# Kernel tuning notes

Hardware: AMD Instinct MI355X
Metric: run time of the kernel (lower is better)

## Reference

```python
import jax, jax.numpy as jnp
import numpy as np

N = 100000
E = 1600000
D_IN = 64
D_H = 64
D_OUT = 10
EPS_BN = 1e-5
EPS_NORM = 1e-12


def setup_inputs() -> dict:
    key = jax.random.key(0)
    ks = jax.random.split(key, 16)
    x = jax.random.normal(ks[0], (N, D_IN), dtype=jnp.float32)
    edge_index = jax.random.randint(ks[1], (2, E), 0, N, dtype=jnp.int64)
    def lin(k, fo, fi):
        s = 1.0 / np.sqrt(fi)
        return jax.random.uniform(k, (fo, fi), jnp.float32, -s, s)
    return {
        "x": x, "edge_index": edge_index,
        "Wl1": lin(ks[2], D_H, D_IN), "Wr1": lin(ks[3], D_H, D_IN), "b1": jnp.zeros((D_H,), jnp.float32),
        "g1": jnp.ones((D_H,), jnp.float32), "be1": jnp.zeros((D_H,), jnp.float32),
        "Wl2": lin(ks[4], D_H, D_H), "Wr2": lin(ks[5], D_H, D_H), "b2": jnp.zeros((D_H,), jnp.float32),
        "g2": jnp.ones((D_H,), jnp.float32), "be2": jnp.zeros((D_H,), jnp.float32),
        "Wl3": lin(ks[6], D_OUT, D_H), "Wr3": lin(ks[7], D_OUT, D_H), "b3": jnp.zeros((D_OUT,), jnp.float32),
    }


def _sage_conv(x, src, dst, Wl, Wr, b, normalize):
    # mean aggregation over incoming edges (messages flow src -> dst)
    agg = jax.ops.segment_sum(x[src], dst, num_segments=N)
    cnt = jax.ops.segment_sum(jnp.ones((src.shape[0],), x.dtype), dst, num_segments=N)
    mean = agg / jnp.clip(cnt, 1.0)[:, None]
    out = mean @ Wl.T + x @ Wr.T + b
    if normalize:
        nrm = jnp.sqrt(jnp.sum(out * out, axis=-1, keepdims=True))
        out = out / jnp.maximum(nrm, EPS_NORM)
    return out


def _batchnorm(x, gamma, beta):
    mu = jnp.mean(x, axis=0)
    var = jnp.mean((x - mu) ** 2, axis=0)  # biased var (training mode)
    return (x - mu) * jax.lax.rsqrt(var + EPS_BN) * gamma + beta


def reference(x, edge_index, Wl1, Wr1, b1, g1, be1, Wl2, Wr2, b2, g2, be2, Wl3, Wr3, b3):
    src, dst = edge_index[0], edge_index[1]
    h = _sage_conv(x, src, dst, Wl1, Wr1, b1, True)
    h = jax.nn.relu(_batchnorm(h, g1, be1))
    h = _sage_conv(h, src, dst, Wl2, Wr2, b2, True)
    h = jax.nn.relu(_batchnorm(h, g2, be2))
    h = _sage_conv(h, src, dst, Wl3, Wr3, b3, False)
    return h
```

## Files before the change

kernel.cpp:

```cpp
#include <hip/hip_runtime.h>
#include <hip/hip_bf16.h>

#define NN 100000
#define EE 1600000
#define BSZ 512
#define NBKT 196
#define CHUNK 8192
#define NCH 196

typedef short bf16x8 __attribute__((ext_vector_type(8)));
typedef float f32x4 __attribute__((ext_vector_type(4)));
typedef float f32x2 __attribute__((ext_vector_type(2)));

__device__ inline unsigned short bf16_of(float f) {
    __hip_bfloat16 h = __float2bfloat16(f);
    return *reinterpret_cast<unsigned short*>(&h);
}
__device__ inline unsigned pack2(float a, float b) {
    return (unsigned)bf16_of(a) | ((unsigned)bf16_of(b) << 16);
}
__device__ inline float bflo(unsigned u) { return __uint_as_float(u << 16); }
__device__ inline float bfhi(unsigned u) { return __uint_as_float(u & 0xffff0000u); }
__device__ inline f32x2 unpk2(unsigned u) {
    f32x2 r; r.x = __uint_as_float(u << 16); r.y = __uint_as_float(u & 0xffff0000u);
    return r;
}


__global__ __launch_bounds__(256)
void k_ccount(const int* __restrict__ ei, int* __restrict__ ccount) {
    __shared__ int hist[NBKT];
    int tid = threadIdx.x;
    int e0 = blockIdx.x * CHUNK;
    int e1 = e0 + CHUNK; if (e1 > EE) e1 = EE;
    for (int i = tid; i < NBKT; i += 256) hist[i] = 0;
    __syncthreads();
    for (int e = e0 + tid; e < e1; e += 256)
        atomicAdd(&hist[ei[EE + e] >> 9], 1);
    __syncthreads();
    for (int i = tid; i < NBKT; i += 256)
        if (hist[i]) atomicAdd(&ccount[i], hist[i]);
}

__global__ void k_cscan(const int* __restrict__ ccount, int* __restrict__ cbase,
                        int* __restrict__ gcur) {
    __shared__ int s[256];
    int tid = threadIdx.x;
    int v = (tid < NBKT) ? ccount[tid] : 0;
    s[tid] = v;
    __syncthreads();
    for (int off = 1; off < 256; off <<= 1) {
        int t = (tid >= off) ? s[tid - off] : 0;
        __syncthreads();
        if (tid >= off) s[tid] += t;
        __syncthreads();
    }
    if (tid < NBKT) {
        int excl = s[tid] - v;
        cbase[tid] = excl;
        gcur[tid] = excl;
    }
    if (tid == NBKT - 1) cbase[NBKT] = s[tid];
}

__global__ __launch_bounds__(256)
void k_coarse(const int* __restrict__ ei, int* __restrict__ gcur, int* __restrict__ pairs) {
    __shared__ int hist[NBKT];
    __shared__ int base[NBKT];
    __shared__ int curs[NBKT];
    int tid = threadIdx.x;
    int e0 = blockIdx.x * CHUNK;
    int e1 = e0 + CHUNK; if (e1 > EE) e1 = EE;
    for (int i = tid; i < NBKT; i += 256) hist[i] = 0;
    __syncthreads();
    for (int e = e0 + tid; e < e1; e += 256)
        atomicAdd(&hist[ei[EE + e] >> 9], 1);
    __syncthreads();
    for (int i = tid; i < NBKT; i += 256) {
        base[i] = atomicAdd(&gcur[i], hist[i]);
        curs[i] = 0;
    }
    __syncthreads();
    for (int e = e0 + tid; e < e1; e += 256) {
        int src = ei[e];
        int dst = ei[EE + e];
        int b = dst >> 9;
        int off = atomicAdd(&curs[b], 1);
        pairs[base[b] + off] = (src << 9) | (dst & 511);
    }
}

__global__ __launch_bounds__(512)
void k_fine(const int* __restrict__ cbase, const int* __restrict__ pairs,
            int* __restrict__ rs, int* __restrict__ esrc) {
    __shared__ int deg[BSZ];
    __shared__ int s[BSZ];
    int b = blockIdx.x;
    int n0 = b * BSZ;
    int nlocal = NN - n0; if (nlocal > BSZ) nlocal = BSZ;
    int tid = threadIdx.x;
    deg[tid] = 0;
    __syncthreads();
    int e0 = cbase[b], e1 = cbase[b + 1];
    for (int e = e0 + tid; e < e1; e += 512)
        atomicAdd(&deg[pairs[e] & 511], 1);
    __syncthreads();
    int v = deg[tid];
    s[tid] = v;
    __syncthreads();
    for (int off = 1; off < 512; off <<= 1) {
        int t = (tid >= off) ? s[tid - off] : 0;
        __syncthreads();
        if (tid >= off) s[tid] += t;
        __syncthreads();
    }
    int excl = s[tid] - v;
    if (tid < nlocal) rs[n0 + tid] = e0 + excl;
    if (b == NBKT - 1 && tid == 0) rs[NN] = EE;
    deg[tid] = e0 + excl;
    __syncthreads();
    for (int e = e0 + tid; e < e1; e += 512) {
        int pk = pairs[e];
        int pos = atomicAdd(&deg[pk & 511], 1);
        esrc[pos] = pk >> 9;
    }
}

__global__ __launch_bounds__(256)
void k_tobfW(const float4* __restrict__ src, ushort4* __restrict__ dst,
             const float* __restrict__ Wl1, const float* __restrict__ Wr1,
             const float* __restrict__ Wl2, const float* __restrict__ Wr2,
             unsigned short* __restrict__ w1, unsigned short* __restrict__ w2,
             int* __restrict__ ccount) {
    int b = blockIdx.x, tid = threadIdx.x;
    if (b < 6250) {
        int i = b * 256 + tid;
        if (i < NN * 16) {
            float4 v = src[i];
            dst[i] = make_ushort4(bf16_of(v.x), bf16_of(v.y), bf16_of(v.z), bf16_of(v.w));
        }
    } else {
        for (int i = tid; i < 8192; i += 256) {
            int n = i >> 7, k = i & 127;
            float v1 = (k < 64) ? Wl1[n * 64 + k] : Wr1[n * 64 + (k - 64)];
            w1[i] = bf16_of(v1);
            float v2 = (k < 64) ? Wl2[n * 64 + k] : Wr2[n * 64 + (k - 64)];
            w2[i] = bf16_of(v2);
        }
        if (tid < NBKT) ccount[tid] = 0;
    }
}

__global__ __launch_bounds__(256, 8)
void k_aggbf(const unsigned short* __restrict__ xbf, const int* __restrict__ rs,
             const int* __restrict__ esrc, unsigned short* __restrict__ meanbf,
             const float* __restrict__ sc, const float* __restrict__ sh) {
    const int tid = threadIdx.x;
    const int node = blockIdx.x * 32 + (tid >> 3);
    if (node >= NN) return;
    const int c = tid & 7;
    const int s0 = rs[node], s1 = rs[node + 1];
    const uint4* xb = (const uint4*)xbf;
    f32x2 a0 = {0.f, 0.f}, a1 = a0, a2 = a0, a3 = a0;
    if (sc) {
        const f32x2* sc2 = (const f32x2*)sc;
        const f32x2* sh2 = (const f32x2*)sh;
        const f32x2 s0v = sc2[4 * c + 0], s1v = sc2[4 * c + 1];
        const f32x2 s2v = sc2[4 * c + 2], s3v = sc2[4 * c + 3];
        const f32x2 h0v = sh2[4 * c + 0], h1v = sh2[4 * c + 1];
        const f32x2 h2v = sh2[4 * c + 2], h3v = sh2[4 * c + 3];
        const f32x2 z = {0.f, 0.f};
#define ACCS(v) do { \
        a0 += __builtin_elementwise_max(__builtin_elementwise_fma(unpk2((v).x), s0v, h0v), z); \
        a1 += __builtin_elementwise_max(__builtin_elementwise_fma(unpk2((v).y), s1v, h1v), z); \
        a2 += __builtin_elementwise_max(__builtin_elementwise_fma(unpk2((v).z), s2v, h2v), z); \
        a3 += __builtin_elementwise_max(__builtin_elementwise_fma(unpk2((v).w), s3v, h3v), z); \
        } while (0)
        int p = s0;
        for (; p + 3 < s1; p += 4) {
            int e0 = esrc[p], e1 = esrc[p + 1], e2 = esrc[p + 2], e3 = esrc[p + 3];
            uint4 v0 = xb[(size_t)e0 * 8 + c];
            uint4 v1 = xb[(size_t)e1 * 8 + c];
            uint4 v2 = xb[(size_t)e2 * 8 + c];
            uint4 v3 = xb[(size_t)e3 * 8 + c];
            ACCS(v0); ACCS(v1); ACCS(v2); ACCS(v3);
        }
        for (; p < s1; ++p) {
            uint4 v = xb[(size_t)esrc[p] * 8 + c];
            ACCS(v);
        }
#undef ACCS
    } else {
#define ACCA(v) do { \
        a0 += unpk2((v).x); a1 += unpk2((v).y); \
        a2 += unpk2((v).z); a3 += unpk2((v).w); } while (0)
        int p = s0;
        for (; p + 3 < s1; p += 4) {
            int e0 = esrc[p], e1 = esrc[p + 1], e2 = esrc[p + 2], e3 = esrc[p + 3];
            uint4 v0 = xb[(size_t)e0 * 8 + c];
            uint4 v1 = xb[(size_t)e1 * 8 + c];
            uint4 v2 = xb[(size_t)e2 * 8 + c];
            uint4 v3 = xb[(size_t)e3 * 8 + c];
            ACCA(v0); ACCA(v1); ACCA(v2); ACCA(v3);
        }
        for (; p < s1; ++p) {
            uint4 v = xb[(size_t)esrc[p] * 8 + c];
            ACCA(v);
        }
#undef ACCA
    }
    int cnt = s1 - s0; if (cnt < 1) cnt = 1;
    float inv = 1.0f / (float)cnt;
    uint4 o;
    o.x = pack2(a0.x * inv, a0.y * inv);
    o.y = pack2(a1.x * inv, a1.y * inv);
    o.z = pack2(a2.x * inv, a2.y * inv);
    o.w = pack2(a3.x * inv, a3.y * inv);
    ((uint4*)meanbf)[(size_t)node * 8 + c] = o;
}

__global__ __launch_bounds__(256, 4)
void k_sagemfma(const unsigned short* __restrict__ meanbf,
                const unsigned short* __restrict__ a2bf,
                const unsigned short* __restrict__ Wbf,
                const float* __restrict__ bias,
                unsigned short* __restrict__ outbf,
                float* __restrict__ partials,
                const float* __restrict__ sc, const float* __restrict__ sh) {
    __shared__ float sblk[64];
    __shared__ float qblk[64];
    const int tid = threadIdx.x;
    const int base = blockIdx.x * 64;
    const int col = tid & 15;
    const int q   = (tid >> 4) & 3;
    const int w   = tid >> 6;

    if (tid < 64) { sblk[tid] = 0.f; qblk[tid] = 0.f; }

    int gn = base + w * 16 + col; if (gn > NN - 1) gn = NN - 1;
    const uint4* mb = (const uint4*)meanbf;
    const uint4* ab = (const uint4*)a2bf;
    const uint4* wb = (const uint4*)Wbf;

    uint4 fa0 = mb[gn * 8 + q];
    uint4 fa1 = mb[gn * 8 + 4 + q];
    uint4 fa2 = ab[gn * 8 + q];
    uint4 fa3 = ab[gn * 8 + 4 + q];
    if (sc) {
        float4 s0 = ((const float4*)sc)[q * 2],     s1 = ((const float4*)sc)[q * 2 + 1];
        float4 h0 = ((const float4*)sh)[q * 2],     h1 = ((const float4*)sh)[q * 2 + 1];
        float4 s2 = ((const float4*)sc)[8 + q * 2], s3 = ((const float4*)sc)[8 + q * 2 + 1];
        float4 h2 = ((const float4*)sh)[8 + q * 2], h3 = ((const float4*)sh)[8 + q * 2 + 1];
        fa2.x = pack2(fmaxf(fmaf(bflo(fa2.x), s0.x, h0.x), 0.f),
                      fmaxf(fmaf(bfhi(fa2.x), s0.y, h0.y), 0.f));
        fa2.y = pack2(fmaxf(fmaf(bflo(fa2.y), s0.z, h0.z), 0.f),
                      fmaxf(fmaf(bfhi(fa2.y), s0.w, h0.w), 0.f));
        fa2.z = pack2(fmaxf(fmaf(bflo(fa2.z), s1.x, h1.x), 0.f),
                      fmaxf(fmaf(bfhi(fa2.z), s1.y, h1.y), 0.f));
        fa2.w = pack2(fmaxf(fmaf(bflo(fa2.w), s1.z, h1.z), 0.f),
                      fmaxf(fmaf(bfhi(fa2.w), s1.w, h1.w), 0.f));
        fa3.x = pack2(fmaxf(fmaf(bflo(fa3.x), s2.x, h2.x), 0.f),
                      fmaxf(fmaf(bfhi(fa3.x), s2.y, h2.y), 0.f));
        fa3.y = pack2(fmaxf(fmaf(bflo(fa3.y), s2.z, h2.z), 0.f),
                      fmaxf(fmaf(bfhi(fa3.y), s2.w, h2.w), 0.f));
        fa3.z = pack2(fmaxf(fmaf(bflo(fa3.z), s3.x, h3.x), 0.f),
                      fmaxf(fmaf(bfhi(fa3.z), s3.y, h3.y), 0.f));
        fa3.w = pack2(fmaxf(fmaf(bflo(fa3.w), s3.z, h3.z), 0.f),
                      fmaxf(fmaf(bfhi(fa3.w), s3.w, h3.w), 0.f));
    }
    uint4 fa[4] = {fa0, fa1, fa2, fa3};

    f32x4 acc0 = {0.f, 0.f, 0.f, 0.f}, acc1 = acc0, acc2 = acc0, acc3 = acc0;
#pragma unroll
    for (int c = 0; c < 4; ++c) {
        uint4 b0 = wb[(0 * 16 + col) * 16 + c * 4 + q];
        uint4 b1 = wb[(1 * 16 + col) * 16 + c * 4 + q];
        uint4 b2 = wb[(2 * 16 + col) * 16 + c * 4 + q];
        uint4 b3 = wb[(3 * 16 + col) * 16 + c * 4 + q];
        bf16x8 a = *(const bf16x8*)&fa[c];
        acc0 = __builtin_amdgcn_mfma_f32_16x16x32_bf16(a, *(const bf16x8*)&b0, acc0, 0, 0, 0);
        acc1 = __builtin_amdgcn_mfma_f32_16x16x32_bf16(a, *(const bf16x8*)&b1, acc1, 0, 0, 0);
        acc2 = __builtin_amdgcn_mfma_f32_16x16x32_bf16(a, *(const bf16x8*)&b2, acc2, 0, 0, 0);
        acc3 = __builtin_amdgcn_mfma_f32_16x16x32_bf16(a, *(const bf16x8*)&b3, acc3, 0, 0, 0);
    }

    float bb0 = bias[col], bb1 = bias[16 + col], bb2 = bias[32 + col], bb3 = bias[48 + col];
    float sj0 = 0.f, sj1 = 0.f, sj2 = 0.f, sj3 = 0.f;
    float qj0 = 0.f, qj1 = 0.f, qj2 = 0.f, qj3 = 0.f;
#pragma unroll
    for (int r = 0; r < 4; ++r) {
        int go = base + w * 16 + q * 4 + r;
        float o0 = acc0[r] + bb0, o1 = acc1[r] + bb1;
        float o2 = acc2[r] + bb2, o3 = acc3[r] + bb3;
        float ssv = o0 * o0 + o1 * o1 + o2 * o2 + o3 * o3;
        ssv += __shfl_xor(ssv, 1, 64);
        ssv += __shfl_xor(ssv, 2, 64);
        ssv += __shfl_xor(ssv, 4, 64);
        ssv += __shfl_xor(ssv, 8, 64);
        float inv = 1.0f / fmaxf(sqrtf(ssv), 1e-12f);
        o0 *= inv; o1 *= inv; o2 *= inv; o3 *= inv;
        if (go < NN) {
            outbf[go * 64 + col]      = bf16_of(o0);
            outbf[go * 64 + 16 + col] = bf16_of(o1);
            outbf[go * 64 + 32 + col] = bf16_of(o2);
            outbf[go * 64 + 48 + col] = bf16_of(o3);
            sj0 += o0; sj1 += o1; sj2 += o2; sj3 += o3;
            qj0 += o0 * o0; qj1 += o1 * o1; qj2 += o2 * o2; qj3 += o3 * o3;
        }
    }
#pragma unroll
    for (int m = 16; m <= 32; m <<= 1) {
        sj0 += __shfl_xor(sj0, m, 64); sj1 += __shfl_xor(sj1, m, 64);
        sj2 += __shfl_xor(sj2, m, 64); sj3 += __shfl_xor(sj3, m, 64);
        qj0 += __shfl_xor(qj0, m, 64); qj1 += __shfl_xor(qj1, m, 64);
        qj2 += __shfl_xor(qj2, m, 64); qj3 += __shfl_xor(qj3, m, 64);
    }
    __syncthreads();
    if (q == 0) {
        atomicAdd(&sblk[col], sj0);      atomicAdd(&qblk[col], qj0);
        atomicAdd(&sblk[16 + col], sj1); atomicAdd(&qblk[16 + col], qj1);
        atomicAdd(&sblk[32 + col], sj2); atomicAdd(&qblk[32 + col], qj2);
        atomicAdd(&sblk[48 + col], sj3); atomicAdd(&qblk[48 + col], qj3);
    }
    __syncthreads();
    if (tid < 128)
        partials[blockIdx.x * 128 + tid] = (tid < 64) ? sblk[tid] : qblk[tid - 64];
}

__global__ __launch_bounds__(256)
void k_bnred(const float* __restrict__ partials, int nblk, float* __restrict__ red) {
    __shared__ float s[256];
    int tid = threadIdx.x;
    int idx = tid & 127, half = tid >> 7;
    float a0 = 0.f, a1 = 0.f, a2 = 0.f, a3 = 0.f;
    int r = blockIdx.x * 2 + half;
    for (; r + 192 < nblk; r += 256) {
        a0 += partials[r * 128 + idx];
        a1 += partials[(r + 64) * 128 + idx];
        a2 += partials[(r + 128) * 128 + idx];
        a3 += partials[(r + 192) * 128 + idx];
    }
    for (; r < nblk; r += 64) a0 += partials[r * 128 + idx];
    s[tid] = (a0 + a1) + (a2 + a3);
    __syncthreads();
    if (tid < 128) red[blockIdx.x * 128 + tid] = s[tid] + s[tid + 128];
}

__global__ void k_bnfin(const float* __restrict__ red,
                        const float* __restrict__ g, const float* __restrict__ be,
                        float* __restrict__ scale, float* __restrict__ shift) {
    __shared__ float s[256];
    int tid = threadIdx.x;
    int idx = tid & 127, half = tid >> 7;
    float a = 0.f;
#pragma unroll
    for (int r = half; r < 32; r += 2)
        a += red[r * 128 + idx];
    s[tid] = a;
    __syncthreads();
    if (tid < 128) s[tid] += s[tid + 128];
    __syncthreads();
    if (tid < 64) {
        float mu = s[tid] / (float)NN;
        float var = s[64 + tid] / (float)NN - mu * mu;
        var = fmaxf(var, 0.0f);
        float sc = g[tid] / sqrtf(var + 1e-5f);
        scale[tid] = sc;
        shift[tid] = be[tid] - mu * sc;
    }
}

__global__ __launch_bounds__(256)
void k_project(const unsigned short* __restrict__ h,
               const float* __restrict__ sc, const float* __restrict__ sh,
               const float* __restrict__ Wl, const float* __restrict__ Wr,
               const float* __restrict__ bias,
               float* __restrict__ zl, float* __restrict__ zr) {
    __shared__ float Alds[64 * 128];
    __shared__ float Wlds[64 * 32];
    const int tid = threadIdx.x;
    const int base = blockIdx.x * 128;

#pragma unroll
    for (int i = 0; i < 8; ++i) {
        int idx = i * 256 + tid;
        int f = idx & 31, k = idx >> 5;
        float v = 0.0f;
        if (f < 16) { if (f < 10) v = Wl[f * 64 + k]; }
        else        { if (f - 16 < 10) v = Wr[(f - 16) * 64 + k]; }
        Wlds[k * 32 + f] = v;
    }
    {
        const uint4* h4 = (const uint4*)h;
        const float4* sc4p = (const float4*)sc;
        const float4* sh4p = (const float4*)sh;
#pragma unroll
        for (int i = 0; i < 4; ++i) {
            int idx = i * 256 + tid;
            int node = idx & 127, cb = idx >> 7;
            int gn = base + node; if (gn > NN - 1) gn = NN - 1;
            uint4 u = h4[gn * 8 + cb];
            float4 sA = sc4p[cb * 2], sB = sc4p[cb * 2 + 1];
            float4 hA = sh4p[cb * 2], hB = sh4p[cb * 2 + 1];
            int k0 = cb * 8;
            Alds[(k0 + 0) * 128 + node] = fmaxf(fmaf(bflo(u.x), sA.x, hA.x), 0.f);
            Alds[(k0 + 1) * 128 + node] = fmaxf(fmaf(bfhi(u.x), sA.y, hA.y), 0.f);
            Alds[(k0 + 2) * 128 + node] = fmaxf(fmaf(bflo(u.y), sA.z, hA.z), 0.f);
            Alds[(k0 + 3) * 128 + node] = fmaxf(fmaf(bfhi(u.y), sA.w, hA.w), 0.f);
            Alds[(k0 + 4) * 128 + node] = fmaxf(fmaf(bflo(u.z), sB.x, hB.x), 0.f);
            Alds[(k0 + 5) * 128 + node] = fmaxf(fmaf(bfhi(u.z), sB.y, hB.y), 0.f);
            Alds[(k0 + 6) * 128 + node] = fmaxf(fmaf(bflo(u.w), sB.z, hB.z), 0.f);
            Alds[(k0 + 7) * 128 + node] = fmaxf(fmaf(bfhi(u.w), sB.w, hB.w), 0.f);
        }
    }
    __syncthreads();

    const int fg = tid & 7;
    const int ng = tid >> 3;

    float acc[4][4] = {};
#pragma unroll 4
    for (int k = 0; k < 64; ++k) {
        const float4 a = *(const float4*)(Alds + k * 128 + (ng << 2));
        const float4 w = *(const float4*)(Wlds + k * 32 + (fg << 2));
        const float av[4] = {a.x, a.y, a.z, a.w};
        const float wv[4] = {w.x, w.y, w.z, w.w};
#pragma unroll
        for (int i = 0; i < 4; ++i)
#pragma unroll
            for (int j = 0; j < 4; ++j)
                acc[i][j] = fmaf(av[i], wv[j], acc[i][j]);
    }

    if (fg == 3 || fg == 7) return;
    float4* dst = (fg < 4) ? (float4*)zl : (float4*)zr;
    int fq = (fg < 4) ? fg : fg - 4;
    float bx = 0.f, by = 0.f, bz = 0.f, bw = 0.f;
    if (fg >= 4) {
        int f0 = fq * 4;
        bx = (f0 + 0 < 10) ? bias[f0 + 0] : 0.f;
        by = (f0 + 1 < 10) ? bias[f0 + 1] : 0.f;
        bz = (f0 + 2 < 10) ? bias[f0 + 2] : 0.f;
        bw = (f0 + 3 < 10) ? bias[f0 + 3] : 0.f;
    }
#pragma unroll
    for (int i = 0; i < 4; ++i) {
        int gn = base + (ng << 2) + i;
        if (gn < NN)
            dst[gn * 3 + fq] = make_float4(acc[i][0] + bx, acc[i][1] + by,
                                           acc[i][2] + bz, acc[i][3] + bw);
    }
}

__global__ __launch_bounds__(256)
void k_agg10(const int* __restrict__ rs, const int* __restrict__ esrc,
             const float* __restrict__ zl, const float* __restrict__ zr,
             float* __restrict__ out) {
    int gid = blockIdx.x * 256 + threadIdx.x;
    unsigned node = (unsigned)gid / 3u;
    int j = gid - (int)node * 3;
    if (node >= NN) return;
    int s0 = rs[node], s1 = rs[node + 1];
    const float4* zl4 = (const float4*)zl;
    float4 acc = make_float4(0.f, 0.f, 0.f, 0.f);
    int p = s0;
    for (; p + 3 < s1; p += 4) {
        float4 v0 = zl4[esrc[p] * 3 + j];
        float4 v1 = zl4[esrc[p + 1] * 3 + j];
        float4 v2 = zl4[esrc[p + 2] * 3 + j];
        float4 v3 = zl4[esrc[p + 3] * 3 + j];
        acc.x += (v0.x + v1.x) + (v2.x + v3.x);
        acc.y += (v0.y + v1.y) + (v2.y + v3.y);
        acc.z += (v0.z + v1.z) + (v2.z + v3.z);
        acc.w += (v0.w + v1.w) + (v2.w + v3.w);
    }
    for (; p < s1; ++p) {
        float4 v = zl4[esrc[p] * 3 + j];
        acc.x += v.x; acc.y += v.y; acc.z += v.z; acc.w += v.w;
    }
    int cnt = s1 - s0; if (cnt < 1) cnt = 1;
    float inv = 1.0f / (float)cnt;
    float4 r = ((const float4*)zr)[node * 3 + j];
    r.x = fmaf(acc.x, inv, r.x); r.y = fmaf(acc.y, inv, r.y);
    r.z = fmaf(acc.z, inv, r.z); r.w = fmaf(acc.w, inv, r.w);
    float2* o2 = (float2*)(out + (size_t)node * 10);
    if (j < 2) {
        o2[j * 2 + 0] = make_float2(r.x, r.y);
        o2[j * 2 + 1] = make_float2(r.z, r.w);
    } else {
        o2[4] = make_float2(r.x, r.y);
    }
}


extern "C" void kernel_launch(void* const* d_in, const int* in_sizes, int n_in,
                              void* d_out, int out_size, void* d_ws, size_t ws_size,
                              hipStream_t stream) {
    const float* x   = (const float*)d_in[0];
    const int*   ei  = (const int*)d_in[1];
    const float* Wl1 = (const float*)d_in[2];
    const float* Wr1 = (const float*)d_in[3];
    const float* b1  = (const float*)d_in[4];
    const float* g1  = (const float*)d_in[5];
    const float* be1 = (const float*)d_in[6];
    const float* Wl2 = (const float*)d_in[7];
    const float* Wr2 = (const float*)d_in[8];
    const float* b2  = (const float*)d_in[9];
    const float* g2  = (const float*)d_in[10];
    const float* be2 = (const float*)d_in[11];
    const float* Wl3 = (const float*)d_in[12];
    const float* Wr3 = (const float*)d_in[13];
    const float* b3  = (const float*)d_in[14];
    float* out = (float*)d_out;

    char* w = (char*)d_ws;
    auto alloc = [&](size_t bytes) -> void* {
        void* p = (void*)w;
        w += (bytes + 255) & ~(size_t)255;
        return p;
    };
    int*   ccount = (int*)alloc(256 * 4);
    int*   cbase  = (int*)alloc(256 * 4);
    int*   gcur   = (int*)alloc(256 * 4);
    int*   rs     = (int*)alloc((size_t)(NN + 1) * 4);
    int*   esrc   = (int*)alloc((size_t)EE * 4);
    float* scratch= (float*)alloc((size_t)NN * 64 * 4);
    unsigned short* xbf    = (unsigned short*)alloc((size_t)NN * 64 * 2);
    unsigned short* h1bf   = (unsigned short*)alloc((size_t)NN * 64 * 2);
    unsigned short* meanbf = (unsigned short*)alloc((size_t)NN * 64 * 2);
    unsigned short* wbf1   = (unsigned short*)alloc(8192 * 2);
    unsigned short* wbf2   = (unsigned short*)alloc(8192 * 2);
    float* partials = (float*)alloc((size_t)1563 * 128 * 4);
    float* red    = (float*)alloc(32 * 128 * 4);
    float* scsh   = (float*)alloc(256 * 4);
    int*   pairs  = (int*)scratch;
    float* zl     = scratch;
    float* zr     = scratch + (size_t)NN * 12;

    k_tobfW<<<6251, 256, 0, stream>>>((const float4*)x, (ushort4*)xbf,
                                      Wl1, Wr1, Wl2, Wr2, wbf1, wbf2, ccount);
    k_ccount<<<NCH, 256, 0, stream>>>(ei, ccount);
    k_cscan<<<1, 256, 0, stream>>>(ccount, cbase, gcur);
    k_coarse<<<NCH, 256, 0, stream>>>(ei, gcur, pairs);
    k_fine<<<NBKT, 512, 0, stream>>>(cbase, pairs, rs, esrc);

    const int aggBlocks  = (NN + 31) / 32;
    const int sageBlocks = (NN + 63) / 64;
    const int projBlocks = (NN + 127) / 128;
    const int a10Blocks  = (NN * 3 + 255) / 256;

    k_aggbf<<<aggBlocks, 256, 0, stream>>>(xbf, rs, esrc, meanbf, nullptr, nullptr);
    k_sagemfma<<<sageBlocks, 256, 0, stream>>>(meanbf, xbf, wbf1, b1, h1bf,
                                               partials, nullptr, nullptr);
    k_bnred<<<32, 256, 0, stream>>>(partials, sageBlocks, red);
    k_bnfin<<<1, 256, 0, stream>>>(red, g1, be1, scsh + 0, scsh + 64);

    k_aggbf<<<aggBlocks, 256, 0, stream>>>(h1bf, rs, esrc, meanbf, scsh + 0, scsh + 64);
    k_sagemfma<<<sageBlocks, 256, 0, stream>>>(meanbf, h1bf, wbf2, b2, xbf,
                                               partials, scsh + 0, scsh + 64);
    k_bnred<<<32, 256, 0, stream>>>(partials, sageBlocks, red);
    k_bnfin<<<1, 256, 0, stream>>>(red, g2, be2, scsh + 128, scsh + 192);

    k_project<<<projBlocks, 256, 0, stream>>>(xbf, scsh + 128, scsh + 192,
                                              Wl3, Wr3, b3, zl, zr);
    k_agg10<<<a10Blocks, 256, 0, stream>>>(rs, esrc, zl, zr, out);
}
```

Baseline: 317.0 us.

## Fuse neighbor mean aggregation into the SAGE MFMA kernel

Result: no change. 320.5 us (+1.1%).

```diff
diff --git a/kernel.cpp b/kernel.cpp
--- a/kernel.cpp
+++ b/kernel.cpp
@@ -151,82 +151,15 @@
     }
 }
 
-__global__ __launch_bounds__(256, 8)
-void k_aggbf(const unsigned short* __restrict__ xbf, const int* __restrict__ rs,
-             const int* __restrict__ esrc, unsigned short* __restrict__ meanbf,
-             const float* __restrict__ sc, const float* __restrict__ sh) {
-    const int tid = threadIdx.x;
-    const int node = blockIdx.x * 32 + (tid >> 3);
-    if (node >= NN) return;
-    const int c = tid & 7;
-    const int s0 = rs[node], s1 = rs[node + 1];
-    const uint4* xb = (const uint4*)xbf;
-    f32x2 a0 = {0.f, 0.f}, a1 = a0, a2 = a0, a3 = a0;
-    if (sc) {
-        const f32x2* sc2 = (const f32x2*)sc;
-        const f32x2* sh2 = (const f32x2*)sh;
-        const f32x2 s0v = sc2[4 * c + 0], s1v = sc2[4 * c + 1];
-        const f32x2 s2v = sc2[4 * c + 2], s3v = sc2[4 * c + 3];
-        const f32x2 h0v = sh2[4 * c + 0], h1v = sh2[4 * c + 1];
-        const f32x2 h2v = sh2[4 * c + 2], h3v = sh2[4 * c + 3];
-        const f32x2 z = {0.f, 0.f};
-#define ACCS(v) do { \
-        a0 += __builtin_elementwise_max(__builtin_elementwise_fma(unpk2((v).x), s0v, h0v), z); \
-        a1 += __builtin_elementwise_max(__builtin_elementwise_fma(unpk2((v).y), s1v, h1v), z); \
-        a2 += __builtin_elementwise_max(__builtin_elementwise_fma(unpk2((v).z), s2v, h2v), z); \
-        a3 += __builtin_elementwise_max(__builtin_elementwise_fma(unpk2((v).w), s3v, h3v), z); \
-        } while (0)
-        int p = s0;
-        for (; p + 3 < s1; p += 4) {
-            int e0 = esrc[p], e1 = esrc[p + 1], e2 = esrc[p + 2], e3 = esrc[p + 3];
-            uint4 v0 = xb[(size_t)e0 * 8 + c];
-            uint4 v1 = xb[(size_t)e1 * 8 + c];
-            uint4 v2 = xb[(size_t)e2 * 8 + c];
-            uint4 v3 = xb[(size_t)e3 * 8 + c];
-            ACCS(v0); ACCS(v1); ACCS(v2); ACCS(v3);
-        }
-        for (; p < s1; ++p) {
-            uint4 v = xb[(size_t)esrc[p] * 8 + c];
-            ACCS(v);
-        }
-#undef ACCS
-    } else {
-#define ACCA(v) do { \
-        a0 += unpk2((v).x); a1 += unpk2((v).y); \
-        a2 += unpk2((v).z); a3 += unpk2((v).w); } while (0)
-        int p = s0;
-        for (; p + 3 < s1; p += 4) {
-            int e0 = esrc[p], e1 = esrc[p + 1], e2 = esrc[p + 2], e3 = esrc[p + 3];
-            uint4 v0 = xb[(size_t)e0 * 8 + c];
-            uint4 v1 = xb[(size_t)e1 * 8 + c];
-            uint4 v2 = xb[(size_t)e2 * 8 + c];
-            uint4 v3 = xb[(size_t)e3 * 8 + c];
-            ACCA(v0); ACCA(v1); ACCA(v2); ACCA(v3);
-        }
-        for (; p < s1; ++p) {
-            uint4 v = xb[(size_t)esrc[p] * 8 + c];
-            ACCA(v);
-        }
-#undef ACCA
-    }
-    int cnt = s1 - s0; if (cnt < 1) cnt = 1;
-    float inv = 1.0f / (float)cnt;
-    uint4 o;
-    o.x = pack2(a0.x * inv, a0.y * inv);
-    o.y = pack2(a1.x * inv, a1.y * inv);
-    o.z = pack2(a2.x * inv, a2.y * inv);
-    o.w = pack2(a3.x * inv, a3.y * inv);
-    ((uint4*)meanbf)[(size_t)node * 8 + c] = o;
-}
-
 __global__ __launch_bounds__(256, 4)
-void k_sagemfma(const unsigned short* __restrict__ meanbf,
-                const unsigned short* __restrict__ a2bf,
-                const unsigned short* __restrict__ Wbf,
-                const float* __restrict__ bias,
-                unsigned short* __restrict__ outbf,
-                float* __restrict__ partials,
-                const float* __restrict__ sc, const float* __restrict__ sh) {
+void k_sagefused(const unsigned short* __restrict__ gtab,
+                 const int* __restrict__ rs, const int* __restrict__ esrc,
+                 const unsigned short* __restrict__ a2bf,
+                 const unsigned short* __restrict__ Wbf,
+                 const float* __restrict__ bias,
+                 unsigned short* __restrict__ outbf,
+                 float* __restrict__ partials,
+                 const float* __restrict__ sc, const float* __restrict__ sh) {
     __shared__ float sblk[64];
     __shared__ float qblk[64];
     const int tid = threadIdx.x;
@@ -238,12 +171,85 @@
     if (tid < 64) { sblk[tid] = 0.f; qblk[tid] = 0.f; }
 
     int gn = base + w * 16 + col; if (gn > NN - 1) gn = NN - 1;
-    const uint4* mb = (const uint4*)meanbf;
+    const uint4* xb = (const uint4*)gtab;
     const uint4* ab = (const uint4*)a2bf;
     const uint4* wb = (const uint4*)Wbf;
 
-    uint4 fa0 = mb[gn * 8 + q];
-    uint4 fa1 = mb[gn * 8 + 4 + q];
+    const int s0e = rs[gn], s1e = rs[gn + 1];
+    const int oA = q, oB = q + 4;
+    f32x2 aA0 = {0.f, 0.f}, aA1 = aA0, aA2 = aA0, aA3 = aA0;
+    f32x2 aB0 = aA0, aB1 = aA0, aB2 = aA0, aB3 = aA0;
+    if (sc) {
+        const f32x2* sc2 = (const f32x2*)sc;
+        const f32x2* sh2 = (const f32x2*)sh;
+        const f32x2 sA0 = sc2[4 * oA + 0], sA1 = sc2[4 * oA + 1];
+        const f32x2 sA2 = sc2[4 * oA + 2], sA3 = sc2[4 * oA + 3];
+        const f32x2 hA0 = sh2[4 * oA + 0], hA1 = sh2[4 * oA + 1];
+        const f32x2 hA2 = sh2[4 * oA + 2], hA3 = sh2[4 * oA + 3];
+        const f32x2 sB0 = sc2[4 * oB + 0], sB1 = sc2[4 * oB + 1];
+        const f32x2 sB2 = sc2[4 * oB + 2], sB3 = sc2[4 * oB + 3];
+        const f32x2 hB0 = sh2[4 * oB + 0], hB1 = sh2[4 * oB + 1];
+        const f32x2 hB2 = sh2[4 * oB + 2], hB3 = sh2[4 * oB + 3];
+        const f32x2 z = {0.f, 0.f};
+#define ACC2S(vA, vB) do { \
+        aA0 += __builtin_elementwise_max(__builtin_elementwise_fma(unpk2((vA).x), sA0, hA0), z); \
+        aA1 += __builtin_elementwise_max(__builtin_elementwise_fma(unpk2((vA).y), sA1, hA1), z); \
+        aA2 += __builtin_elementwise_max(__builtin_elementwise_fma(unpk2((vA).z), sA2, hA2), z); \
+        aA3 += __builtin_elementwise_max(__builtin_elementwise_fma(unpk2((vA).w), sA3, hA3), z); \
+        aB0 += __builtin_elementwise_max(__builtin_elementwise_fma(unpk2((vB).x), sB0, hB0), z); \
+        aB1 += __builtin_elementwise_max(__builtin_elementwise_fma(unpk2((vB).y), sB1, hB1), z); \
+        aB2 += __builtin_elementwise_max(__builtin_elementwise_fma(unpk2((vB).z), sB2, hB2), z); \
+        aB3 += __builtin_elementwise_max(__builtin_elementwise_fma(unpk2((vB).w), sB3, hB3), z); \
+        } while (0)
+        int p = s0e;
+        for (; p + 3 < s1e; p += 4) {
+            int e0 = esrc[p], e1 = esrc[p + 1], e2 = esrc[p + 2], e3 = esrc[p + 3];
+            uint4 vA0 = xb[(size_t)e0 * 8 + oA]; uint4 vB0 = xb[(size_t)e0 * 8 + oB];
+            uint4 vA1 = xb[(size_t)e1 * 8 + oA]; uint4 vB1 = xb[(size_t)e1 * 8 + oB];
+            uint4 vA2 = xb[(size_t)e2 * 8 + oA]; uint4 vB2 = xb[(size_t)e2 * 8 + oB];
+            uint4 vA3 = xb[(size_t)e3 * 8 + oA]; uint4 vB3 = xb[(size_t)e3 * 8 + oB];
+            ACC2S(vA0, vB0); ACC2S(vA1, vB1); ACC2S(vA2, vB2); ACC2S(vA3, vB3);
+        }
+        for (; p < s1e; ++p) {
+            uint4 vA = xb[(size_t)esrc[p] * 8 + oA];
+            uint4 vB = xb[(size_t)esrc[p] * 8 + oB];
+            ACC2S(vA, vB);
+        }
+#undef ACC2S
+    } else {
+#define ACC2A(vA, vB) do { \
+        aA0 += unpk2((vA).x); aA1 += unpk2((vA).y); \
+        aA2 += unpk2((vA).z); aA3 += unpk2((vA).w); \
+        aB0 += unpk2((vB).x); aB1 += unpk2((vB).y); \
+        aB2 += unpk2((vB).z); aB3 += unpk2((vB).w); } while (0)
+        int p = s0e;
+        for (; p + 3 < s1e; p += 4) {
+            int e0 = esrc[p], e1 = esrc[p + 1], e2 = esrc[p + 2], e3 = esrc[p + 3];
+            uint4 vA0 = xb[(size_t)e0 * 8 + oA]; uint4 vB0 = xb[(size_t)e0 * 8 + oB];
+            uint4 vA1 = xb[(size_t)e1 * 8 + oA]; uint4 vB1 = xb[(size_t)e1 * 8 + oB];
+            uint4 vA2 = xb[(size_t)e2 * 8 + oA]; uint4 vB2 = xb[(size_t)e2 * 8 + oB];
+            uint4 vA3 = xb[(size_t)e3 * 8 + oA]; uint4 vB3 = xb[(size_t)e3 * 8 + oB];
+            ACC2A(vA0, vB0); ACC2A(vA1, vB1); ACC2A(vA2, vB2); ACC2A(vA3, vB3);
+        }
+        for (; p < s1e; ++p) {
+            uint4 vA = xb[(size_t)esrc[p] * 8 + oA];
+            uint4 vB = xb[(size_t)esrc[p] * 8 + oB];
+            ACC2A(vA, vB);
+        }
+#undef ACC2A
+    }
+    int cnt = s1e - s0e; if (cnt < 1) cnt = 1;
+    float inv = 1.0f / (float)cnt;
+    uint4 fa0, fa1;
+    fa0.x = pack2(aA0.x * inv, aA0.y * inv);
+    fa0.y = pack2(aA1.x * inv, aA1.y * inv);
+    fa0.z = pack2(aA2.x * inv, aA2.y * inv);
+    fa0.w = pack2(aA3.x * inv, aA3.y * inv);
+    fa1.x = pack2(aB0.x * inv, aB0.y * inv);
+    fa1.y = pack2(aB1.x * inv, aB1.y * inv);
+    fa1.z = pack2(aB2.x * inv, aB2.y * inv);
+    fa1.w = pack2(aB3.x * inv, aB3.y * inv);
+
     uint4 fa2 = ab[gn * 8 + q];
     uint4 fa3 = ab[gn * 8 + 4 + q];
     if (sc) {
@@ -297,8 +303,8 @@
         ssv += __shfl_xor(ssv, 2, 64);
         ssv += __shfl_xor(ssv, 4, 64);
         ssv += __shfl_xor(ssv, 8, 64);
-        float inv = 1.0f / fmaxf(sqrtf(ssv), 1e-12f);
-        o0 *= inv; o1 *= inv; o2 *= inv; o3 *= inv;
+        float inv2 = 1.0f / fmaxf(sqrtf(ssv), 1e-12f);
+        o0 *= inv2; o1 *= inv2; o2 *= inv2; o3 *= inv2;
         if (go < NN) {
             outbf[go * 64 + col]      = bf16_of(o0);
             outbf[go * 64 + 16 + col] = bf16_of(o1);
@@ -527,7 +533,6 @@
     float* scratch= (float*)alloc((size_t)NN * 64 * 4);
     unsigned short* xbf    = (unsigned short*)alloc((size_t)NN * 64 * 2);
     unsigned short* h1bf   = (unsigned short*)alloc((size_t)NN * 64 * 2);
-    unsigned short* meanbf = (unsigned short*)alloc((size_t)NN * 64 * 2);
     unsigned short* wbf1   = (unsigned short*)alloc(8192 * 2);
     unsigned short* wbf2   = (unsigned short*)alloc(8192 * 2);
     float* partials = (float*)alloc((size_t)1563 * 128 * 4);
@@ -544,20 +549,17 @@
     k_coarse<<<NCH, 256, 0, stream>>>(ei, gcur, pairs);
     k_fine<<<NBKT, 512, 0, stream>>>(cbase, pairs, rs, esrc);
 
-    const int aggBlocks  = (NN + 31) / 32;
     const int sageBlocks = (NN + 63) / 64;
     const int projBlocks = (NN + 127) / 128;
     const int a10Blocks  = (NN * 3 + 255) / 256;
 
-    k_aggbf<<<aggBlocks, 256, 0, stream>>>(xbf, rs, esrc, meanbf, nullptr, nullptr);
-    k_sagemfma<<<sageBlocks, 256, 0, stream>>>(meanbf, xbf, wbf1, b1, h1bf,
-                                               partials, nullptr, nullptr);
+    k_sagefused<<<sageBlocks, 256, 0, stream>>>(xbf, rs, esrc, xbf, wbf1, b1, h1bf,
+                                                partials, nullptr, nullptr);
     k_bnred<<<32, 256, 0, stream>>>(partials, sageBlocks, red);
     k_bnfin<<<1, 256, 0, stream>>>(red, g1, be1, scsh + 0, scsh + 64);
 
-    k_aggbf<<<aggBlocks, 256, 0, stream>>>(h1bf, rs, esrc, meanbf, scsh + 0, scsh + 64);
-    k_sagemfma<<<sageBlocks, 256, 0, stream>>>(meanbf, h1bf, wbf2, b2, xbf,
-                                               partials, scsh + 0, scsh + 64);
+    k_sagefused<<<sageBlocks, 256, 0, stream>>>(h1bf, rs, esrc, h1bf, wbf2, b2, xbf,
+                                                partials, scsh + 0, scsh + 64);
     k_bnred<<<32, 256, 0, stream>>>(partials, sageBlocks, red);
     k_bnfin<<<1, 256, 0, stream>>>(red, g2, be2, scsh + 128, scsh + 192);
 
```

## Stage coarse bucket scatter in LDS and unroll gather loop by eight

Applied to the files above, without the earlier changes.

Measured after the change: 325.4 us. 2.7% more time.

```diff
diff --git a/kernel.cpp b/kernel.cpp
--- a/kernel.cpp
+++ b/kernel.cpp
@@ -66,27 +66,50 @@
 __global__ __launch_bounds__(256)
 void k_coarse(const int* __restrict__ ei, int* __restrict__ gcur, int* __restrict__ pairs) {
     __shared__ int hist[NBKT];
-    __shared__ int base[NBKT];
+    __shared__ int lbase[NBKT];
+    __shared__ int gbase[NBKT];
     __shared__ int curs[NBKT];
+    __shared__ int plds[CHUNK];
+    __shared__ unsigned char blds[CHUNK];
+    __shared__ int s[256];
     int tid = threadIdx.x;
     int e0 = blockIdx.x * CHUNK;
     int e1 = e0 + CHUNK; if (e1 > EE) e1 = EE;
-    for (int i = tid; i < NBKT; i += 256) hist[i] = 0;
+    int n = e1 - e0;
+    for (int i = tid; i < NBKT; i += 256) { hist[i] = 0; curs[i] = 0; }
     __syncthreads();
     for (int e = e0 + tid; e < e1; e += 256)
         atomicAdd(&hist[ei[EE + e] >> 9], 1);
     __syncthreads();
-    for (int i = tid; i < NBKT; i += 256) {
-        base[i] = atomicAdd(&gcur[i], hist[i]);
-        curs[i] = 0;
-    }
+    {
+        int v = (tid < NBKT) ? hist[tid] : 0;
+        s[tid] = v;
+        __syncthreads();
+        for (int off = 1; off < 256; off <<= 1) {
+            int t = (tid >= off) ? s[tid - off] : 0;
+            __syncthreads();
+            if (tid >= off) s[tid] += t;
+            __syncthreads();
+        }
+        if (tid < NBKT) lbase[tid] = s[tid] - v;
+    }
+    __syncthreads();
+    for (int i = tid; i < NBKT; i += 256)
+        gbase[i] = atomicAdd(&gcur[i], hist[i]);
     __syncthreads();
     for (int e = e0 + tid; e < e1; e += 256) {
         int src = ei[e];
         int dst = ei[EE + e];
         int b = dst >> 9;
         int off = atomicAdd(&curs[b], 1);
-        pairs[base[b] + off] = (src << 9) | (dst & 511);
+        int li = lbase[b] + off;
+        plds[li] = (src << 9) | (dst & 511);
+        blds[li] = (unsigned char)b;
+    }
+    __syncthreads();
+    for (int i = tid; i < n; i += 256) {
+        int b = blds[i];
+        pairs[gbase[b] + (i - lbase[b])] = plds[i];
     }
 }
 
@@ -177,6 +200,20 @@
         a3 += __builtin_elementwise_max(__builtin_elementwise_fma(unpk2((v).w), s3v, h3v), z); \
         } while (0)
         int p = s0;
+        for (; p + 7 < s1; p += 8) {
+            int e0 = esrc[p],     e1 = esrc[p + 1], e2 = esrc[p + 2], e3 = esrc[p + 3];
+            int e4 = esrc[p + 4], e5 = esrc[p + 5], e6 = esrc[p + 6], e7 = esrc[p + 7];
+            uint4 v0 = xb[(size_t)e0 * 8 + c];
+            uint4 v1 = xb[(size_t)e1 * 8 + c];
+            uint4 v2 = xb[(size_t)e2 * 8 + c];
+            uint4 v3 = xb[(size_t)e3 * 8 + c];
+            uint4 v4 = xb[(size_t)e4 * 8 + c];
+            uint4 v5 = xb[(size_t)e5 * 8 + c];
+            uint4 v6 = xb[(size_t)e6 * 8 + c];
+            uint4 v7 = xb[(size_t)e7 * 8 + c];
+            ACCS(v0); ACCS(v1); ACCS(v2); ACCS(v3);
+            ACCS(v4); ACCS(v5); ACCS(v6); ACCS(v7);
+        }
         for (; p + 3 < s1; p += 4) {
             int e0 = esrc[p], e1 = esrc[p + 1], e2 = esrc[p + 2], e3 = esrc[p + 3];
             uint4 v0 = xb[(size_t)e0 * 8 + c];
@@ -195,6 +232,20 @@
         a0 += unpk2((v).x); a1 += unpk2((v).y); \
         a2 += unpk2((v).z); a3 += unpk2((v).w); } while (0)
         int p = s0;
+        for (; p + 7 < s1; p += 8) {
+            int e0 = esrc[p],     e1 = esrc[p + 1], e2 = esrc[p + 2], e3 = esrc[p + 3];
+            int e4 = esrc[p + 4], e5 = esrc[p + 5], e6 = esrc[p + 6], e7 = esrc[p + 7];
+            uint4 v0 = xb[(size_t)e0 * 8 + c];
+            uint4 v1 = xb[(size_t)e1 * 8 + c];
+            uint4 v2 = xb[(size_t)e2 * 8 + c];
+            uint4 v3 = xb[(size_t)e3 * 8 + c];
+            uint4 v4 = xb[(size_t)e4 * 8 + c];
+            uint4 v5 = xb[(size_t)e5 * 8 + c];
+            uint4 v6 = xb[(size_t)e6 * 8 + c];
+            uint4 v7 = xb[(size_t)e7 * 8 + c];
+            ACCA(v0); ACCA(v1); ACCA(v2); ACCA(v3);
+            ACCA(v4); ACCA(v5); ACCA(v6); ACCA(v7);
+        }
         for (; p + 3 < s1; p += 4) {
             int e0 = esrc[p], e1 = esrc[p + 1], e2 = esrc[p + 2], e3 = esrc[p + 3];
             uint4 v0 = xb[(size_t)e0 * 8 + c];
```

## Fuse histogram into conversion kernel, per-chunk bases, atomic BN reduction

Applied to the files above, without the earlier changes.

Measured after the change: 304.6 us. -3.9%, faster.

```diff
diff --git a/kernel.cpp b/kernel.cpp
--- a/kernel.cpp
+++ b/kernel.cpp
@@ -26,28 +26,50 @@
     return r;
 }
 
-
 __global__ __launch_bounds__(256)
-void k_ccount(const int* __restrict__ ei, int* __restrict__ ccount) {
-    __shared__ int hist[NBKT];
-    int tid = threadIdx.x;
-    int e0 = blockIdx.x * CHUNK;
-    int e1 = e0 + CHUNK; if (e1 > EE) e1 = EE;
-    for (int i = tid; i < NBKT; i += 256) hist[i] = 0;
-    __syncthreads();
-    for (int e = e0 + tid; e < e1; e += 256)
-        atomicAdd(&hist[ei[EE + e] >> 9], 1);
-    __syncthreads();
-    for (int i = tid; i < NBKT; i += 256)
-        if (hist[i]) atomicAdd(&ccount[i], hist[i]);
-}
-
-__global__ void k_cscan(const int* __restrict__ ccount, int* __restrict__ cbase,
-                        int* __restrict__ gcur) {
+void k_tobfW(const float4* __restrict__ src, ushort4* __restrict__ dst,
+             const float* __restrict__ Wl1, const float* __restrict__ Wr1,
+             const float* __restrict__ Wl2, const float* __restrict__ Wr2,
+             unsigned short* __restrict__ w1, unsigned short* __restrict__ w2,
+             const int* __restrict__ ei, int* __restrict__ chunkhist,
+             float* __restrict__ bnacc1) {
+    int b = blockIdx.x, tid = threadIdx.x;
+    if (b < 6250) {
+        int i = b * 256 + tid;
+        float4 v = src[i];
+        dst[i] = make_ushort4(bf16_of(v.x), bf16_of(v.y), bf16_of(v.z), bf16_of(v.w));
+    } else if (b == 6250) {
+        for (int i = tid; i < 8192; i += 256) {
+            int n = i >> 7, k = i & 127;
+            float v1 = (k < 64) ? Wl1[n * 64 + k] : Wr1[n * 64 + (k - 64)];
+            w1[i] = bf16_of(v1);
+            float v2 = (k < 64) ? Wl2[n * 64 + k] : Wr2[n * 64 + (k - 64)];
+            w2[i] = bf16_of(v2);
+        }
+        for (int i = tid; i < 1024; i += 256) bnacc1[i] = 0.f;
+    } else {
+        __shared__ int hist[NBKT];
+        int ch = b - 6251;
+        int e0 = ch * CHUNK;
+        int e1 = e0 + CHUNK; if (e1 > EE) e1 = EE;
+        for (int i = tid; i < NBKT; i += 256) hist[i] = 0;
+        __syncthreads();
+        for (int e = e0 + tid; e < e1; e += 256)
+            atomicAdd(&hist[ei[EE + e] >> 9], 1);
+        __syncthreads();
+        for (int i = tid; i < NBKT; i += 256)
+            chunkhist[i * NCH + ch] = hist[i];
+    }
+}
+
+__global__ void k_cscan(const int* __restrict__ chunkhist, int* __restrict__ cbase,
+                        int* __restrict__ chunkbase) {
     __shared__ int s[256];
     int tid = threadIdx.x;
-    int v = (tid < NBKT) ? ccount[tid] : 0;
-    s[tid] = v;
+    int total = 0;
+    if (tid < NBKT)
+        for (int ch = 0; ch < NCH; ++ch) total += chunkhist[tid * NCH + ch];
+    s[tid] = total;
     __syncthreads();
     for (int off = 1; off < 256; off <<= 1) {
         int t = (tid >= off) ? s[tid - off] : 0;
@@ -56,28 +78,29 @@
         __syncthreads();
     }
     if (tid < NBKT) {
-        int excl = s[tid] - v;
+        int excl = s[tid] - total;
         cbase[tid] = excl;
-        gcur[tid] = excl;
+        int run = excl;
+        for (int ch = 0; ch < NCH; ++ch) {
+            int t = chunkhist[tid * NCH + ch];
+            chunkbase[tid * NCH + ch] = run;
+            run += t;
+        }
     }
     if (tid == NBKT - 1) cbase[NBKT] = s[tid];
 }
 
 __global__ __launch_bounds__(256)
-void k_coarse(const int* __restrict__ ei, int* __restrict__ gcur, int* __restrict__ pairs) {
-    __shared__ int hist[NBKT];
+void k_coarse(const int* __restrict__ ei, const int* __restrict__ chunkbase,
+              int* __restrict__ pairs) {
     __shared__ int base[NBKT];
     __shared__ int curs[NBKT];
     int tid = threadIdx.x;
-    int e0 = blockIdx.x * CHUNK;
+    int ch = blockIdx.x;
+    int e0 = ch * CHUNK;
     int e1 = e0 + CHUNK; if (e1 > EE) e1 = EE;
-    for (int i = tid; i < NBKT; i += 256) hist[i] = 0;
-    __syncthreads();
-    for (int e = e0 + tid; e < e1; e += 256)
-        atomicAdd(&hist[ei[EE + e] >> 9], 1);
-    __syncthreads();
     for (int i = tid; i < NBKT; i += 256) {
-        base[i] = atomicAdd(&gcur[i], hist[i]);
+        base[i] = chunkbase[i * NCH + ch];
         curs[i] = 0;
     }
     __syncthreads();
@@ -123,31 +146,6 @@
         int pk = pairs[e];
         int pos = atomicAdd(&deg[pk & 511], 1);
         esrc[pos] = pk >> 9;
-    }
-}
-
-__global__ __launch_bounds__(256)
-void k_tobfW(const float4* __restrict__ src, ushort4* __restrict__ dst,
-             const float* __restrict__ Wl1, const float* __restrict__ Wr1,
-             const float* __restrict__ Wl2, const float* __restrict__ Wr2,
-             unsigned short* __restrict__ w1, unsigned short* __restrict__ w2,
-             int* __restrict__ ccount) {
-    int b = blockIdx.x, tid = threadIdx.x;
-    if (b < 6250) {
-        int i = b * 256 + tid;
-        if (i < NN * 16) {
-            float4 v = src[i];
-            dst[i] = make_ushort4(bf16_of(v.x), bf16_of(v.y), bf16_of(v.z), bf16_of(v.w));
-        }
-    } else {
-        for (int i = tid; i < 8192; i += 256) {
-            int n = i >> 7, k = i & 127;
-            float v1 = (k < 64) ? Wl1[n * 64 + k] : Wr1[n * 64 + (k - 64)];
-            w1[i] = bf16_of(v1);
-            float v2 = (k < 64) ? Wl2[n * 64 + k] : Wr2[n * 64 + (k - 64)];
-            w2[i] = bf16_of(v2);
-        }
-        if (tid < NBKT) ccount[tid] = 0;
     }
 }
 
@@ -225,7 +223,7 @@
                 const unsigned short* __restrict__ Wbf,
                 const float* __restrict__ bias,
                 unsigned short* __restrict__ outbf,
-                float* __restrict__ partials,
+                float* __restrict__ bnacc,
                 const float* __restrict__ sc, const float* __restrict__ sh) {
     __shared__ float sblk[64];
     __shared__ float qblk[64];
@@ -324,41 +322,24 @@
     }
     __syncthreads();
     if (tid < 128)
-        partials[blockIdx.x * 128 + tid] = (tid < 64) ? sblk[tid] : qblk[tid - 64];
-}
-
-__global__ __launch_bounds__(256)
-void k_bnred(const float* __restrict__ partials, int nblk, float* __restrict__ red) {
-    __shared__ float s[256];
+        atomicAdd(&bnacc[(blockIdx.x & 7) * 128 + tid],
+                  (tid < 64) ? sblk[tid] : qblk[tid - 64]);
+}
+
+__global__ void k_bnfin(const float* __restrict__ bnacc,
+                        const float* __restrict__ g, const float* __restrict__ be,
+                        float* __restrict__ scale, float* __restrict__ shift,
+                        float* __restrict__ nextacc) {
+    __shared__ float s[128];
     int tid = threadIdx.x;
-    int idx = tid & 127, half = tid >> 7;
-    float a0 = 0.f, a1 = 0.f, a2 = 0.f, a3 = 0.f;
-    int r = blockIdx.x * 2 + half;
-    for (; r + 192 < nblk; r += 256) {
-        a0 += partials[r * 128 + idx];
-        a1 += partials[(r + 64) * 128 + idx];
-        a2 += partials[(r + 128) * 128 + idx];
-        a3 += partials[(r + 192) * 128 + idx];
-    }
-    for (; r < nblk; r += 64) a0 += partials[r * 128 + idx];
-    s[tid] = (a0 + a1) + (a2 + a3);
-    __syncthreads();
-    if (tid < 128) red[blockIdx.x * 128 + tid] = s[tid] + s[tid + 128];
-}
-
-__global__ void k_bnfin(const float* __restrict__ red,
-                        const float* __restrict__ g, const float* __restrict__ be,
-                        float* __restrict__ scale, float* __restrict__ shift) {
-    __shared__ float s[256];
-    int tid = threadIdx.x;
-    int idx = tid & 127, half = tid >> 7;
-    float a = 0.f;
-#pragma unroll
-    for (int r = half; r < 32; r += 2)
-        a += red[r * 128 + idx];
-    s[tid] = a;
-    __syncthreads();
-    if (tid < 128) s[tid] += s[tid + 128];
+    if (tid < 128) {
+        float a = 0.f;
+#pragma unroll
+        for (int r = 0; r < 8; ++r) a += bnacc[r * 128 + tid];
+        s[tid] = a;
+    }
+    if (nextacc)
+        for (int i = tid; i < 1024; i += 256) nextacc[i] = 0.f;
     __syncthreads();
     if (tid < 64) {
         float mu = s[tid] / (float)NN;
@@ -519,9 +500,9 @@
         w += (bytes + 255) & ~(size_t)255;
         return p;
     };
-    int*   ccount = (int*)alloc(256 * 4);
-    int*   cbase  = (int*)alloc(256 * 4);
-    int*   gcur   = (int*)alloc(256 * 4);
+    int*   cbase     = (int*)alloc(256 * 4);
+    int*   chunkhist = (int*)alloc((size_t)NBKT * NCH * 4);
+    int*   chunkbase = (int*)alloc((size_t)NBKT * NCH * 4);
     int*   rs     = (int*)alloc((size_t)(NN + 1) * 4);
     int*   esrc   = (int*)alloc((size_t)EE * 4);
     float* scratch= (float*)alloc((size_t)NN * 64 * 4);
@@ -530,18 +511,18 @@
     unsigned short* meanbf = (unsigned short*)alloc((size_t)NN * 64 * 2);
     unsigned short* wbf1   = (unsigned short*)alloc(8192 * 2);
     unsigned short* wbf2   = (unsigned short*)alloc(8192 * 2);
-    float* partials = (float*)alloc((size_t)1563 * 128 * 4);
-    float* red    = (float*)alloc(32 * 128 * 4);
+    float* bnacc1 = (float*)alloc(1024 * 4);
+    float* bnacc2 = (float*)alloc(1024 * 4);
     float* scsh   = (float*)alloc(256 * 4);
     int*   pairs  = (int*)scratch;
     float* zl     = scratch;
     float* zr     = scratch + (size_t)NN * 12;
 
-    k_tobfW<<<6251, 256, 0, stream>>>((const float4*)x, (ushort4*)xbf,
-                                      Wl1, Wr1, Wl2, Wr2, wbf1, wbf2, ccount);
-    k_ccount<<<NCH, 256, 0, stream>>>(ei, ccount);
-    k_cscan<<<1, 256, 0, stream>>>(ccount, cbase, gcur);
-    k_coarse<<<NCH, 256, 0, stream>>>(ei, gcur, pairs);
+    k_tobfW<<<6251 + NCH, 256, 0, stream>>>((const float4*)x, (ushort4*)xbf,
+                                            Wl1, Wr1, Wl2, Wr2, wbf1, wbf2,
+                                            ei, chunkhist, bnacc1);
+    k_cscan<<<1, 256, 0, stream>>>(chunkhist, cbase, chunkbase);
+    k_coarse<<<NCH, 256, 0, stream>>>(ei, chunkbase, pairs);
     k_fine<<<NBKT, 512, 0, stream>>>(cbase, pairs, rs, esrc);
 
     const int aggBlocks  = (NN + 31) / 32;
@@ -551,15 +532,13 @@
 
     k_aggbf<<<aggBlocks, 256, 0, stream>>>(xbf, rs, esrc, meanbf, nullptr, nullptr);
     k_sagemfma<<<sageBlocks, 256, 0, stream>>>(meanbf, xbf, wbf1, b1, h1bf,
-                                               partials, nullptr, nullptr);
-    k_bnred<<<32, 256, 0, stream>>>(partials, sageBlocks, red);
-    k_bnfin<<<1, 256, 0, stream>>>(red, g1, be1, scsh + 0, scsh + 64);
+                                               bnacc1, nullptr, nullptr);
+    k_bnfin<<<1, 256, 0, stream>>>(bnacc1, g1, be1, scsh + 0, scsh + 64, bnacc2);
 
     k_aggbf<<<aggBlocks, 256, 0, stream>>>(h1bf, rs, esrc, meanbf, scsh + 0, scsh + 64);
     k_sagemfma<<<sageBlocks, 256, 0, stream>>>(meanbf, h1bf, wbf2, b2, xbf,
-                                               partials, scsh + 0, scsh + 64);
-    k_bnred<<<32, 256, 0, stream>>>(partials, sageBlocks, red);
-    k_bnfin<<<1, 256, 0, stream>>>(red, g2, be2, scsh + 128, scsh + 192);
+                                               bnacc2, scsh + 0, scsh + 64);
+    k_bnfin<<<1, 256, 0, stream>>>(bnacc2, g2, be2, scsh + 128, scsh + 192, nullptr);
 
     k_project<<<projBlocks, 256, 0, stream>>>(xbf, scsh + 128, scsh + 192,
                                               Wl3, Wr3, b3, zl, zr);
```
